# Kernel tuning notes

Hardware: AMD Instinct MI355X
Metric: run time of the kernel (lower is better)

Reference implementation:

```python
import jax, jax.numpy as jnp
import numpy as np

N_NODES = 100000
N_EDGES = 3200000
IN_CH = 128
HIDDEN = 16
OUT_CH = 40


def gcn_conv(x, src, dst, norm, W, b, num_nodes):
    # PyG GCNConv: out[i] = sum_{(j->i)} norm_ji * (x @ W)[j] + b
    h = x @ W                      # [N, F_out]
    msg = h[src] * norm[:, None]   # gather + scale, [E', F_out]
    out = jax.ops.segment_sum(msg, dst, num_segments=num_nodes)
    return out + b


def setup_inputs() -> dict:
    key = jax.random.key(0)
    k1, k2, k3, k4, k5 = jax.random.split(key, 5)
    x = jax.random.normal(k1, (N_NODES, IN_CH), dtype=jnp.float32)
    edge_index = jax.random.randint(k2, (2, N_EDGES), 0, N_NODES, dtype=jnp.int64)
    # Glorot-style init for the two GCN layers
    W1 = jax.random.normal(k3, (IN_CH, HIDDEN), dtype=jnp.float32) / np.sqrt(IN_CH)
    b1 = jnp.zeros((HIDDEN,), dtype=jnp.float32)
    W2 = jax.random.normal(k4, (HIDDEN, OUT_CH), dtype=jnp.float32) / np.sqrt(HIDDEN)
    b2 = jnp.zeros((OUT_CH,), dtype=jnp.float32)
    return {"x": x, "edge_index": edge_index, "W1": W1, "b1": b1, "W2": W2, "b2": b2}


def reference(x, edge_index, W1, b1, W2, b2):
    num_nodes = x.shape[0]
    # add self-loops (PyG default add_self_loops=True)
    loop = jnp.arange(num_nodes, dtype=edge_index.dtype)
    src = jnp.concatenate([edge_index[0], loop])
    dst = jnp.concatenate([edge_index[1], loop])
    # symmetric normalization deg^{-1/2}[src] * deg^{-1/2}[dst], deg over in-edges incl. self-loops
    deg = jax.ops.segment_sum(jnp.ones_like(dst, dtype=x.dtype), dst, num_segments=num_nodes)
    dis = jnp.where(deg > 0, jax.lax.rsqrt(jnp.maximum(deg, 1.0)), 0.0)
    norm = dis[src] * dis[dst]     # [E+N]

    h = jax.nn.relu(gcn_conv(x, src, dst, norm, W1, b1, num_nodes))
    out = gcn_conv(h, src, dst, norm, W2, b2, num_nodes)
    return jax.nn.log_softmax(out, axis=1)
```

## Files before the change

### kernel.cpp

```cpp
#include <hip/hip_runtime.h>
#include <math.h>

#define NN 100000
#define NE 3200000
#define INC 128
#define HID 16
#define OC 40

#define NBK 391
#define CAP 8960
#define CSTRIDE 16
#define EB 4096
#define PBLK 782

__device__ __forceinline__ unsigned bf16r(float f) {
    unsigned u = __float_as_uint(f);
    return (u + 0x7FFFu + ((u >> 16) & 1u)) >> 16;
}
__device__ __forceinline__ unsigned packbf(float a, float b) {
    return bf16r(a) | (bf16r(b) << 16);
}
__device__ __forceinline__ float bflo(unsigned u) { return __uint_as_float(u << 16); }
__device__ __forceinline__ float bfhi(unsigned u) { return __uint_as_float(u & 0xFFFF0000u); }

__global__ void k_zero_i(int* __restrict__ p, int n) {
    int i = blockIdx.x * blockDim.x + threadIdx.x;
    if (i < n) p[i] = 0;
}

__global__ __launch_bounds__(512) void k_part(const int* __restrict__ src,
                                              const int* __restrict__ dst,
                                              int* __restrict__ cursor,
                                              int* __restrict__ bin) {
    __shared__ int hist[512];
    __shared__ int pref[512];
    __shared__ int lcur[512];
    __shared__ int gbase[512];
    __shared__ unsigned sorted[EB];
    __shared__ unsigned short sortedb[EB];
    __shared__ int tot_s;
    int t = threadIdx.x;
    int e0 = blockIdx.x * EB;
    int cnt = min(EB, NE - e0);
    hist[t] = 0;
    __syncthreads();
    for (int i = t; i < cnt; i += 512) {
        unsigned d = (unsigned)dst[e0 + i];
        unsigned s = (unsigned)src[e0 + i];
        if (d < NN && s < NN) atomicAdd(&hist[d >> 8], 1);
    }
    __syncthreads();
    pref[t] = hist[t];
    __syncthreads();
    for (int d = 1; d < 512; d <<= 1) {
        int add = (t >= d) ? pref[t - d] : 0;
        __syncthreads();
        pref[t] += add;
        __syncthreads();
    }
    int lst = pref[t] - hist[t];
    lcur[t] = 0;
    pref[t] = lst;
    if (t == 511) tot_s = lst + hist[511];
    if (t < NBK) gbase[t] = atomicAdd(&cursor[t * CSTRIDE], hist[t]);
    __syncthreads();
    for (int i = t; i < cnt; i += 512) {
        unsigned d = (unsigned)dst[e0 + i];
        unsigned s = (unsigned)src[e0 + i];
        if (d < NN && s < NN) {
            int b = (int)(d >> 8);
            int p = atomicAdd(&lcur[b], 1);
            int idx = pref[b] + p;
            sorted[idx] = ((d & 255u) << 17) | s;
            sortedb[idx] = (unsigned short)b;
        }
    }
    __syncthreads();
    int tot = tot_s;
    for (int i = t; i < tot; i += 512) {
        int b = sortedb[i];
        int gp = gbase[b] + (i - pref[b]);
        if (gp < CAP) bin[b * CAP + gp] = (int)sorted[i];
    }
}

__global__ __launch_bounds__(512) void k_bsort(int* __restrict__ bin,
                                               const int* __restrict__ cursor,
                                               int* __restrict__ off,
                                               int* __restrict__ endv,
                                               float* __restrict__ dis) {
    __shared__ int hist[256];
    __shared__ int pref[256];
    __shared__ int lcur[256];
    __shared__ int sorted[CAP];
    int b = blockIdx.x, t = threadIdx.x;
    int cnt = cursor[b * CSTRIDE];
    if (cnt > CAP) cnt = CAP;
    int base = b * CAP;
    if (t < 256) hist[t] = 0;
    __syncthreads();
    for (int i = t; i < cnt; i += 512) {
        unsigned w = (unsigned)bin[base + i];
        atomicAdd(&hist[w >> 17], 1);
    }
    __syncthreads();
    if (t < 256) pref[t] = hist[t];
    __syncthreads();
    for (int d = 1; d < 256; d <<= 1) {
        int add = (t >= d && t < 256) ? pref[t - d] : 0;
        __syncthreads();
        if (t < 256) pref[t] += add;
        __syncthreads();
    }
    if (t < 256) lcur[t] = pref[t] - hist[t];
    __syncthreads();
    for (int i = t; i < cnt; i += 512) {
        unsigned w = (unsigned)bin[base + i];
        int p = atomicAdd(&lcur[w >> 17], 1);
        sorted[p] = (int)(w & 0x1FFFF);
    }
    __syncthreads();
    for (int i = t; i < cnt; i += 512) bin[base + i] = sorted[i];
    if (t < 256) {
        int node = (b << 8) + t;
        if (node < NN) {
            off[node]  = base + pref[t] - hist[t];
            endv[node] = base + pref[t];
            dis[node]  = rsqrtf((float)(hist[t] + 1));
        }
    }
}

__global__ __launch_bounds__(256) void k_gemm1(const float* __restrict__ x,
                                               const float* __restrict__ W1,
                                               const float* __restrict__ dis,
                                               unsigned* __restrict__ g1) {
    __shared__ float xs[16][INC + 1];
    __shared__ float ws[INC][HID];
    __shared__ float accs[16][17];
    int t = threadIdx.x;
    int rowbase = blockIdx.x * 16;
#pragma unroll
    for (int i = 0; i < 8; ++i) {
        int idx = t + i * 256;
        xs[idx >> 7][idx & 127] = x[(long long)(rowbase)*INC + idx];
    }
#pragma unroll
    for (int i = 0; i < 8; ++i) {
        int idx = t + i * 256;
        ws[idx >> 4][idx & 15] = W1[idx];
    }
    __syncthreads();
    int r = t >> 4, c = t & 15;
    float acc = 0.f;
#pragma unroll
    for (int k = 0; k < INC; ++k) acc += xs[r][k] * ws[k][c];
    accs[r][c] = dis[rowbase + r] * acc;
    __syncthreads();
    if (t < 128) {
        int row = t >> 3, p = t & 7;
        g1[(rowbase + row) * 8 + p] = packbf(accs[row][2 * p], accs[row][2 * p + 1]);
    }
}

#define UNPACK4(u, f) \
    f[0] = bflo(u.x); f[1] = bfhi(u.x); f[2] = bflo(u.y); f[3] = bfhi(u.y);

__device__ __forceinline__ void gather_core(const unsigned* __restrict__ gin,
                                            const int* __restrict__ bin,
                                            int node, int c4, int es,
                                            int beg, int end, float di,
                                            float a[4]) {
    const uint2* gv = (const uint2*)gin;
    float f[4];
    if (es == 0) {
        uint2 u = gv[node * 4 + c4];
        UNPACK4(u, a)
    } else {
        a[0] = a[1] = a[2] = a[3] = 0.f;
    }
    int j = beg + es;
    for (; j + 6 < end; j += 8) {
        int s0 = bin[j], s1 = bin[j + 2], s2 = bin[j + 4], s3 = bin[j + 6];
        uint2 u0 = gv[s0 * 4 + c4];
        uint2 u1 = gv[s1 * 4 + c4];
        uint2 u2 = gv[s2 * 4 + c4];
        uint2 u3 = gv[s3 * 4 + c4];
        UNPACK4(u0, f)
#pragma unroll
        for (int k = 0; k < 4; ++k) a[k] += f[k];
        UNPACK4(u1, f)
#pragma unroll
        for (int k = 0; k < 4; ++k) a[k] += f[k];
        UNPACK4(u2, f)
#pragma unroll
        for (int k = 0; k < 4; ++k) a[k] += f[k];
        UNPACK4(u3, f)
#pragma unroll
        for (int k = 0; k < 4; ++k) a[k] += f[k];
    }
    for (; j < end; j += 2) {
        uint2 uu = gv[bin[j] * 4 + c4];
        UNPACK4(uu, f)
#pragma unroll
        for (int k = 0; k < 4; ++k) a[k] += f[k];
    }
#pragma unroll
    for (int k = 0; k < 4; ++k) {
        a[k] += __shfl_xor(a[k], 4);
        a[k] *= di;
    }
}

__global__ __launch_bounds__(256) void k_gather1(const unsigned* __restrict__ gin,
                                                 const float* __restrict__ dis,
                                                 const int* __restrict__ off,
                                                 const int* __restrict__ endv,
                                                 const int* __restrict__ bin,
                                                 const float* __restrict__ bias,
                                                 unsigned* __restrict__ outbf) {
    int t = threadIdx.x;
    int node = blockIdx.x * 32 + (t >> 3);
    if (node >= NN) return;
    int lane3 = t & 7;
    int c4 = lane3 & 3, es = lane3 >> 2;
    float di = dis[node];
    float a[4];
    gather_core(gin, bin, node, c4, es, off[node], endv[node], di, a);
    if (es == 0) {
#pragma unroll
        for (int k = 0; k < 4; ++k)
            a[k] = fmaxf(a[k] + bias[c4 * 4 + k], 0.f) * di;
        uint2 o; o.x = packbf(a[0], a[1]); o.y = packbf(a[2], a[3]);
        ((uint2*)outbf)[node * 4 + c4] = o;
    }
}

__global__ __launch_bounds__(256) void k_gather2(const unsigned* __restrict__ gin,
                                                 const float* __restrict__ dis,
                                                 const int* __restrict__ off,
                                                 const int* __restrict__ endv,
                                                 const int* __restrict__ bin,
                                                 const float* __restrict__ W2,
                                                 const float* __restrict__ b2,
                                                 float* __restrict__ out) {
    __shared__ float accs[32][HID + 1];
    __shared__ float w2s[HID * OC];
    __shared__ float b2s[OC];
    int t = threadIdx.x;
    for (int i = t; i < HID * OC; i += 256) w2s[i] = W2[i];
    if (t < OC) b2s[t] = b2[t];
    int nl = t >> 3;
    int node = blockIdx.x * 32 + nl;
    int lane3 = t & 7;
    int c4 = lane3 & 3, es = lane3 >> 2;
    if (node < NN) {
        float di = dis[node];
        float a[4];
        gather_core(gin, bin, node, c4, es, off[node], endv[node], di, a);
        if (es == 0) {
#pragma unroll
            for (int k = 0; k < 4; ++k) accs[nl][c4 * 4 + k] = a[k];
        }
    }
    __syncthreads();
    if (node >= NN) return;
    float a[HID];
#pragma unroll
    for (int k = 0; k < HID; ++k) a[k] = accs[nl][k];
    float z[5];
#pragma unroll
    for (int j = 0; j < 5; ++j) {
        int c = lane3 * 5 + j;
        float zz = b2s[c];
#pragma unroll
        for (int k = 0; k < HID; ++k) zz += a[k] * w2s[k * OC + c];
        z[j] = zz;
    }
    float m = z[0];
#pragma unroll
    for (int j = 1; j < 5; ++j) m = fmaxf(m, z[j]);
    m = fmaxf(m, __shfl_xor(m, 1));
    m = fmaxf(m, __shfl_xor(m, 2));
    m = fmaxf(m, __shfl_xor(m, 4));
    float s = 0.f;
#pragma unroll
    for (int j = 0; j < 5; ++j) s += expf(z[j] - m);
    s += __shfl_xor(s, 1);
    s += __shfl_xor(s, 2);
    s += __shfl_xor(s, 4);
    float lse = m + logf(s);
    float* op = out + (size_t)node * OC + lane3 * 5;
#pragma unroll
    for (int j = 0; j < 5; ++j) op[j] = z[j] - lse;
}

extern "C" void kernel_launch(void* const* d_in, const int* in_sizes, int n_in,
                              void* d_out, int out_size, void* d_ws, size_t ws_size,
                              hipStream_t stream) {
    const float* x  = (const float*)d_in[0];
    const int*   ei = (const int*)d_in[1];
    const float* W1 = (const float*)d_in[2];
    const float* b1 = (const float*)d_in[3];
    const float* W2 = (const float*)d_in[4];
    const float* b2 = (const float*)d_in[5];
    float* out = (float*)d_out;

    const int* src = ei;
    const int* dst = ei + NE;

    char* ws = (char*)d_ws;
    size_t o = 0;
    int*      cursor = (int*)(ws + o);      o += (size_t)NBK * CSTRIDE * 4;
    float*    dis    = (float*)(ws + o);    o += (size_t)NN * 4;
    int*      off    = (int*)(ws + o);      o += (size_t)NN * 4;
    int*      endv   = (int*)(ws + o);      o += (size_t)NN * 4;
    int*      bin    = (int*)(ws + o);      o += (size_t)NBK * CAP * 4;
    unsigned* gbf1   = (unsigned*)(ws + o); o += (size_t)NN * 8 * 4;
    unsigned* gbf2   = (unsigned*)(ws + o); o += (size_t)NN * 8 * 4;

    dim3 B(256);
    int gC = (NBK * CSTRIDE + 255) / 256;
    int gG = (NN + 31) / 32;

    k_zero_i<<<gC, B, 0, stream>>>(cursor, NBK * CSTRIDE);
    k_part<<<PBLK, 512, 0, stream>>>(src, dst, cursor, bin);
    k_bsort<<<NBK, 512, 0, stream>>>(bin, cursor, off, endv, dis);
    k_gemm1<<<NN / 16, B, 0, stream>>>(x, W1, dis, gbf1);
    k_gather1<<<gG, B, 0, stream>>>(gbf1, dis, off, endv, bin, b1, gbf2);
    k_gather2<<<gG, B, 0, stream>>>(gbf2, dis, off, endv, bin, W2, b2, out);
}
```

Baseline: 134.6 us.

## Use wave-shuffle scans, register-cached edges, float4 loads, and 16 lanes per node

The partition kernel now keeps each thread's edges in registers so src/dst are read once rather than twice. Both partition and bucket-sort kernels replace the log-step shared-memory scan, which needs many barriers, with a wave-level shuffle scan plus a small per-wave base. The first GEMM loads x and W1 as float4 into padded shared memory. The gather kernels use 16 lanes per node (4 edge streams) instead of 8, giving more memory parallelism per node but half as many nodes per block, and add one more shuffle reduction.

```diff
diff --git a/kernel.cpp b/kernel.cpp
--- a/kernel.cpp
+++ b/kernel.cpp
@@ -38,40 +38,60 @@
     __shared__ int gbase[512];
     __shared__ unsigned sorted[EB];
     __shared__ unsigned short sortedb[EB];
+    __shared__ int wsum[8], wbase[8];
     __shared__ int tot_s;
     int t = threadIdx.x;
+    int lane = t & 63, wid = t >> 6;
     int e0 = blockIdx.x * EB;
     int cnt = min(EB, NE - e0);
     hist[t] = 0;
     __syncthreads();
-    for (int i = t; i < cnt; i += 512) {
-        unsigned d = (unsigned)dst[e0 + i];
-        unsigned s = (unsigned)src[e0 + i];
-        if (d < NN && s < NN) atomicAdd(&hist[d >> 8], 1);
-    }
-    __syncthreads();
-    pref[t] = hist[t];
-    __syncthreads();
-    for (int d = 1; d < 512; d <<= 1) {
-        int add = (t >= d) ? pref[t - d] : 0;
-        __syncthreads();
-        pref[t] += add;
-        __syncthreads();
-    }
-    int lst = pref[t] - hist[t];
+    unsigned wreg[8];
+    int breg[8];
+#pragma unroll
+    for (int k = 0; k < 8; ++k) {
+        int i = t + k * 512;
+        breg[k] = -1;
+        if (i < cnt) {
+            unsigned d = (unsigned)dst[e0 + i];
+            unsigned s = (unsigned)src[e0 + i];
+            if (d < NN && s < NN) {
+                breg[k] = (int)(d >> 8);
+                wreg[k] = ((d & 255u) << 17) | s;
+                atomicAdd(&hist[breg[k]], 1);
+            }
+        }
+    }
+    __syncthreads();
+    int v = hist[t];
+    int sv = v;
+#pragma unroll
+    for (int d = 1; d < 64; d <<= 1) {
+        int up = __shfl_up(sv, d);
+        if (lane >= d) sv += up;
+    }
+    if (lane == 63) wsum[wid] = sv;
+    __syncthreads();
+    if (t < 8) {
+        int acc = 0;
+        for (int i = 0; i < t; ++i) acc += wsum[i];
+        wbase[t] = acc;
+    }
+    __syncthreads();
+    int incl = sv + wbase[wid];
+    int excl = incl - v;
+    pref[t] = excl;
     lcur[t] = 0;
-    pref[t] = lst;
-    if (t == 511) tot_s = lst + hist[511];
-    if (t < NBK) gbase[t] = atomicAdd(&cursor[t * CSTRIDE], hist[t]);
-    __syncthreads();
-    for (int i = t; i < cnt; i += 512) {
-        unsigned d = (unsigned)dst[e0 + i];
-        unsigned s = (unsigned)src[e0 + i];
-        if (d < NN && s < NN) {
-            int b = (int)(d >> 8);
+    if (t == 511) tot_s = incl;
+    if (t < NBK) gbase[t] = atomicAdd(&cursor[t * CSTRIDE], v);
+    __syncthreads();
+#pragma unroll
+    for (int k = 0; k < 8; ++k) {
+        if (breg[k] >= 0) {
+            int b = breg[k];
             int p = atomicAdd(&lcur[b], 1);
             int idx = pref[b] + p;
-            sorted[idx] = ((d & 255u) << 17) | s;
+            sorted[idx] = wreg[k];
             sortedb[idx] = (unsigned short)b;
         }
     }
@@ -93,6 +113,7 @@
     __shared__ int pref[256];
     __shared__ int lcur[256];
     __shared__ int sorted[CAP];
+    __shared__ int wsum[4], wbase[4];
     int b = blockIdx.x, t = threadIdx.x;
     int cnt = cursor[b * CSTRIDE];
     if (cnt > CAP) cnt = CAP;
@@ -104,15 +125,30 @@
         atomicAdd(&hist[w >> 17], 1);
     }
     __syncthreads();
-    if (t < 256) pref[t] = hist[t];
-    __syncthreads();
-    for (int d = 1; d < 256; d <<= 1) {
-        int add = (t >= d && t < 256) ? pref[t - d] : 0;
-        __syncthreads();
-        if (t < 256) pref[t] += add;
-        __syncthreads();
-    }
-    if (t < 256) lcur[t] = pref[t] - hist[t];
+    int v = 0, sv = 0;
+    if (t < 256) {
+        v = hist[t];
+        sv = v;
+        int lane = t & 63;
+#pragma unroll
+        for (int d = 1; d < 64; d <<= 1) {
+            int up = __shfl_up(sv, d);
+            if (lane >= d) sv += up;
+        }
+        if (lane == 63) wsum[t >> 6] = sv;
+    }
+    __syncthreads();
+    if (t < 4) {
+        int acc = 0;
+        for (int i = 0; i < t; ++i) acc += wsum[i];
+        wbase[t] = acc;
+    }
+    __syncthreads();
+    if (t < 256) {
+        int incl = sv + wbase[t >> 6];
+        pref[t] = incl;
+        lcur[t] = incl - v;
+    }
     __syncthreads();
     for (int i = t; i < cnt; i += 512) {
         unsigned w = (unsigned)bin[base + i];
@@ -135,20 +171,24 @@
                                                const float* __restrict__ W1,
                                                const float* __restrict__ dis,
                                                unsigned* __restrict__ g1) {
-    __shared__ float xs[16][INC + 1];
+    __shared__ float xs[16][132];
     __shared__ float ws[INC][HID];
     __shared__ float accs[16][17];
     int t = threadIdx.x;
     int rowbase = blockIdx.x * 16;
-#pragma unroll
-    for (int i = 0; i < 8; ++i) {
+    const float4* x4 = (const float4*)(x + (size_t)rowbase * INC);
+#pragma unroll
+    for (int i = 0; i < 2; ++i) {
         int idx = t + i * 256;
-        xs[idx >> 7][idx & 127] = x[(long long)(rowbase)*INC + idx];
-    }
-#pragma unroll
-    for (int i = 0; i < 8; ++i) {
+        float4 vv = x4[idx];
+        *(float4*)&xs[idx >> 5][(idx & 31) * 4] = vv;
+    }
+    const float4* w4 = (const float4*)W1;
+#pragma unroll
+    for (int i = 0; i < 2; ++i) {
         int idx = t + i * 256;
-        ws[idx >> 4][idx & 15] = W1[idx];
+        float4 vv = w4[idx];
+        *(float4*)&ws[idx >> 2][(idx & 3) * 4] = vv;
     }
     __syncthreads();
     int r = t >> 4, c = t & 15;
@@ -180,8 +220,8 @@
         a[0] = a[1] = a[2] = a[3] = 0.f;
     }
     int j = beg + es;
-    for (; j + 6 < end; j += 8) {
-        int s0 = bin[j], s1 = bin[j + 2], s2 = bin[j + 4], s3 = bin[j + 6];
+    for (; j + 12 < end; j += 16) {
+        int s0 = bin[j], s1 = bin[j + 4], s2 = bin[j + 8], s3 = bin[j + 12];
         uint2 u0 = gv[s0 * 4 + c4];
         uint2 u1 = gv[s1 * 4 + c4];
         uint2 u2 = gv[s2 * 4 + c4];
@@ -199,7 +239,7 @@
 #pragma unroll
         for (int k = 0; k < 4; ++k) a[k] += f[k];
     }
-    for (; j < end; j += 2) {
+    for (; j < end; j += 4) {
         uint2 uu = gv[bin[j] * 4 + c4];
         UNPACK4(uu, f)
 #pragma unroll
@@ -208,6 +248,7 @@
 #pragma unroll
     for (int k = 0; k < 4; ++k) {
         a[k] += __shfl_xor(a[k], 4);
+        a[k] += __shfl_xor(a[k], 8);
         a[k] *= di;
     }
 }
@@ -220,10 +261,10 @@
                                                  const float* __restrict__ bias,
                                                  unsigned* __restrict__ outbf) {
     int t = threadIdx.x;
-    int node = blockIdx.x * 32 + (t >> 3);
+    int node = blockIdx.x * 16 + (t >> 4);
     if (node >= NN) return;
-    int lane3 = t & 7;
-    int c4 = lane3 & 3, es = lane3 >> 2;
+    int lane4 = t & 15;
+    int c4 = lane4 & 3, es = lane4 >> 2;
     float di = dis[node];
     float a[4];
     gather_core(gin, bin, node, c4, es, off[node], endv[node], di, a);
@@ -244,16 +285,16 @@
                                                  const float* __restrict__ W2,
                                                  const float* __restrict__ b2,
                                                  float* __restrict__ out) {
-    __shared__ float accs[32][HID + 1];
+    __shared__ float accs[16][HID + 1];
     __shared__ float w2s[HID * OC];
     __shared__ float b2s[OC];
     int t = threadIdx.x;
     for (int i = t; i < HID * OC; i += 256) w2s[i] = W2[i];
     if (t < OC) b2s[t] = b2[t];
-    int nl = t >> 3;
-    int node = blockIdx.x * 32 + nl;
-    int lane3 = t & 7;
-    int c4 = lane3 & 3, es = lane3 >> 2;
+    int nl = t >> 4;
+    int node = blockIdx.x * 16 + nl;
+    int lane4 = t & 15;
+    int c4 = lane4 & 3, es = lane4 >> 2;
     if (node < NN) {
         float di = dis[node];
         float a[4];
@@ -264,14 +305,14 @@
         }
     }
     __syncthreads();
-    if (node >= NN) return;
+    if (node >= NN || lane4 >= 8) return;
     float a[HID];
 #pragma unroll
     for (int k = 0; k < HID; ++k) a[k] = accs[nl][k];
     float z[5];
 #pragma unroll
     for (int j = 0; j < 5; ++j) {
-        int c = lane3 * 5 + j;
+        int c = lane4 * 5 + j;
         float zz = b2s[c];
 #pragma unroll
         for (int k = 0; k < HID; ++k) zz += a[k] * w2s[k * OC + c];
@@ -290,7 +331,7 @@
     s += __shfl_xor(s, 2);
     s += __shfl_xor(s, 4);
     float lse = m + logf(s);
-    float* op = out + (size_t)node * OC + lane3 * 5;
+    float* op = out + (size_t)node * OC + lane4 * 5;
 #pragma unroll
     for (int j = 0; j < 5; ++j) op[j] = z[j] - lse;
 }
@@ -321,7 +362,7 @@
 
     dim3 B(256);
     int gC = (NBK * CSTRIDE + 255) / 256;
-    int gG = (NN + 31) / 32;
+    int gG = (NN + 15) / 16;
 
     k_zero_i<<<gC, B, 0, stream>>>(cursor, NBK * CSTRIDE);
     k_part<<<PBLK, 512, 0, stream>>>(src, dst, cursor, bin);
```

Measured after the change: 126.0 us. 1.07x faster.
